# Kernel optimization log

Measured on AMD Instinct MI355X. Metric: run time of the kernel, lower is better.

The kernel has to match this reference:

```python
import jax, jax.numpy as jnp
import numpy as np

N = 1_000_000
C = 32
DIMS = (480, 360, 32)  # cylindrical voxel grid (z/rho, phi, height)
EPS = 1e-5


def setup_inputs() -> dict:
    rng = np.random.default_rng(0)
    total = DIMS[0] * DIMS[1] * DIMS[2]
    # unique active voxels, sorted so searchsorted gives row indices directly
    ids = np.sort(rng.choice(total, size=N, replace=False)).astype(np.int64)
    z = ids // (DIMS[1] * DIMS[2])
    rem = ids % (DIMS[1] * DIMS[2])
    y = rem // DIMS[2]
    x = rem % DIMS[2]
    coords = np.stack([z, y, x], axis=1)
    strides = np.array([DIMS[1] * DIMS[2], DIMS[2], 1], dtype=np.int64)

    def nbr(delta):
        out = np.full((3, N), -1, dtype=np.int32)
        for a in range(3):
            tgt = ids + delta * strides[a]
            ok = (coords[:, a] + delta >= 0) & (coords[:, a] + delta < DIMS[a])
            pos = np.searchsorted(ids, tgt)
            pos_c = np.clip(pos, 0, N - 1)
            found = ok & (ids[pos_c] == tgt)
            out[a] = np.where(found, pos_c, -1).astype(np.int32)
        return out

    nbr_prev = nbr(-1)
    nbr_next = nbr(+1)

    key = jax.random.key(0)
    k0, k1, k2 = jax.random.split(key, 3)
    features = jax.random.normal(k0, (N, C), dtype=jnp.float32)
    # W[branch, tap, in, out]; taps ordered (-1, 0, +1) along the branch's axis
    W = jax.random.normal(k1, (3, 3, C, C), dtype=jnp.float32) * (1.0 / np.sqrt(3 * C))
    gamma = jnp.ones((3, C), dtype=jnp.float32)
    beta = jnp.zeros((3, C), dtype=jnp.float32)
    mean = jax.random.normal(k2, (3, C), dtype=jnp.float32) * 0.1
    var = jnp.ones((3, C), dtype=jnp.float32)
    return {
        "features": features,
        "nbr_prev": jnp.asarray(nbr_prev),
        "nbr_next": jnp.asarray(nbr_next),
        "W": W,
        "gamma": gamma,
        "beta": beta,
        "mean": mean,
        "var": var,
    }


def _branch(f, Wb, prev, nxt, g, b, m, v):
    # 3-tap submanifold conv along one axis: gather prev/next active neighbors
    pm = prev >= 0
    nm = nxt >= 0
    fp = jnp.where(pm[:, None], f[jnp.where(pm, prev, 0)], 0.0)
    fn = jnp.where(nm[:, None], f[jnp.where(nm, nxt, 0)], 0.0)
    out = fp @ Wb[0] + f @ Wb[1] + fn @ Wb[2]
    # BatchNorm1d (inference stats) + Sigmoid
    out = (out - m) * (g * jax.lax.rsqrt(v + EPS)) + b
    return jax.nn.sigmoid(out)


def reference(features, nbr_prev, nbr_next, W, gamma, beta, mean, var):
    acc = jnp.zeros_like(features)
    for a in range(3):  # conv3x1x1, conv1x3x1, conv1x1x3
        acc = acc + _branch(features, W[a], nbr_prev[a], nbr_next[a],
                            gamma[a], beta[a], mean[a], var[a])
    return acc * features  # sparse_add then gating with input features
```

## Files before the change

kernel.cpp:

```cpp
#include <hip/hip_runtime.h>
#include <stdint.h>


typedef __attribute__((ext_vector_type(8))) __bf16 bf16x8;
typedef __attribute__((ext_vector_type(8))) unsigned short u16x8;
typedef __attribute__((ext_vector_type(4))) float f32x4;
typedef __attribute__((ext_vector_type(2))) float f32x2;

constexpr int NVOX    = 1000000;
constexpr int NTILES  = NVOX / 16;
constexpr int WPB     = 4;
constexpr float LOG2E = 1.4426950408889634f;

constexpr int TPWF     = 5;
constexpr int NWAVESF  = NTILES / TPWF;
constexpr int NBLOCKSF = NWAVESF / WPB;

constexpr int TPW2     = 2;
constexpr int NWAVES2  = (NTILES + TPW2 - 1) / TPW2;
constexpr int NBLOCKS2 = (NWAVES2 + WPB - 1) / WPB;

constexpr int    WS_WELEMS = 18 * 64 * 8;
constexpr size_t FB_BYTES  = (size_t)NVOX * 64;
constexpr unsigned ZOFF    = (unsigned)(FB_BYTES + 18432 + 768);
constexpr size_t WS_NEED   = FB_BYTES + 18432 + 768 + 128;

constexpr int CVT_THREADS = NVOX * 32 / 16;
constexpr int PREP_TAIL   = WS_WELEMS + 96 + 32;
constexpr int PREPALL_BLK = (CVT_THREADS + PREP_TAIL + 255) / 256;

__device__ __forceinline__ unsigned pack_bf(float a, float b) {
    union { float f; unsigned u; } ca, cb; ca.f = a; cb.f = b;
    return __builtin_amdgcn_perm(cb.u + 0x8000u, ca.u + 0x8000u, 0x07060302u);
}

__device__ __forceinline__ void prep_tail_work(
    int t, const float* __restrict__ Wt,
    const float* __restrict__ gma, const float* __restrict__ bta,
    const float* __restrict__ mea, const float* __restrict__ var,
    unsigned short* __restrict__ wsW, float* __restrict__ wsA,
    float* __restrict__ wsB, float* __restrict__ wsZ)
{
    if (t < WS_WELEMS) {
        int f    = t >> 9;
        int rem  = t & 511;
        int lane = rem >> 3;
        int j    = rem & 7;
        int br = f / 6, tap = (f >> 1) % 3, h = f & 1;
        int n = lane & 15, quad = lane >> 4;
        float w = Wt[((br * 3 + tap) * 32 + quad * 8 + j) * 32 + 2 * n + h];
        union { float f; unsigned u; } c; c.f = w;
        wsW[(f * 64 + lane) * 8 + j] = (unsigned short)((c.u + 0x8000u) >> 16);
    } else if (t < WS_WELEMS + 96) {
        int i = t - WS_WELEMS;
        float s = gma[i] * __frsqrt_rn(var[i] + 1e-5f);
        wsA[i] = -s * LOG2E;
        wsB[i] = (mea[i] * s - bta[i]) * LOG2E;
    } else if (wsZ != nullptr && t < WS_WELEMS + 96 + 32) {
        wsZ[t - WS_WELEMS - 96] = 0.0f;
    }
}

__global__ __launch_bounds__(256) void prep_all(
    const float* __restrict__ feat, unsigned short* __restrict__ fb,
    const float* __restrict__ Wt,
    const float* __restrict__ gma, const float* __restrict__ bta,
    const float* __restrict__ mea, const float* __restrict__ var,
    unsigned short* __restrict__ wsW, float* __restrict__ wsA,
    float* __restrict__ wsB, float* __restrict__ wsZ)
{
    int tid = blockIdx.x * 256 + threadIdx.x;
    if (tid < CVT_THREADS) {
        const f32x4* p = (const f32x4*)(feat + (size_t)tid * 16);
        f32x4 v0 = p[0], v1 = p[1], v2 = p[2], v3 = p[3];
        union { unsigned u[8]; u16x8 v[2]; } r;
        r.u[0] = pack_bf(v0[0], v0[1]); r.u[1] = pack_bf(v0[2], v0[3]);
        r.u[2] = pack_bf(v1[0], v1[1]); r.u[3] = pack_bf(v1[2], v1[3]);
        r.u[4] = pack_bf(v2[0], v2[1]); r.u[5] = pack_bf(v2[2], v2[3]);
        r.u[6] = pack_bf(v3[0], v3[1]); r.u[7] = pack_bf(v3[2], v3[3]);
        u16x8* q = (u16x8*)(fb + (size_t)tid * 16);
        q[0] = r.v[0]; q[1] = r.v[1];
    } else {
        prep_tail_work(tid - CVT_THREADS, Wt, gma, bta, mea, var,
                       wsW, wsA, wsB, wsZ);
    }
}

__global__ __launch_bounds__(256) void prep_kernel(
    const float* __restrict__ Wt,
    const float* __restrict__ gma, const float* __restrict__ bta,
    const float* __restrict__ mea, const float* __restrict__ var,
    unsigned short* __restrict__ wsW, float* __restrict__ wsA,
    float* __restrict__ wsB)
{
    int tid = blockIdx.x * 256 + threadIdx.x;
    prep_tail_work(tid, Wt, gma, bta, mea, var, wsW, wsA, wsB, nullptr);
}

__device__ __forceinline__ bf16x8 cvt_frag(f32x4 lo, f32x4 hi) {
    union { unsigned u[4]; bf16x8 v; } r;
    r.u[0] = pack_bf(lo[0], lo[1]); r.u[1] = pack_bf(lo[2], lo[3]);
    r.u[2] = pack_bf(hi[0], hi[1]); r.u[3] = pack_bf(hi[2], hi[3]);
    return r.v;
}

__device__ __forceinline__ f32x4 mfma16(u16x8 a, bf16x8 b, f32x4 c) {
    return __builtin_amdgcn_mfma_f32_16x16x32_bf16(
        __builtin_bit_cast(bf16x8, a), b, c, 0, 0, 0);
}

__global__ __launch_bounds__(256) void recon_bf16(
    const float* __restrict__ feat,
    const int*   __restrict__ nprev,
    const int*   __restrict__ nnext,
    const char*  __restrict__ fbc,
    const unsigned short* __restrict__ wsW,
    const float* __restrict__ wsA,
    const float* __restrict__ wsB,
    float*       __restrict__ out)
{
    __shared__ unsigned short smem[WS_WELEMS];
    {
        const u16x8* s = (const u16x8*)wsW;
        u16x8* d = (u16x8*)smem;
        #pragma unroll
        for (int i = 0; i < 5; ++i) {
            int k = (int)threadIdx.x + i * 256;
            if (k < 18 * 64) d[k] = s[k];
        }
    }
    __syncthreads();

    const int lane = threadIdx.x & 63;
    const int n    = lane & 15;
    const int quad = lane >> 4;
    const unsigned qo = (unsigned)quad * 16u;

    int b   = blockIdx.x;
    int per = NBLOCKSF / 8;
    int bs  = (b < per * 8) ? ((b & 7) * per + (b >> 3)) : b;
    int wv  = bs * WPB + (threadIdx.x >> 6);
    if (wv >= NWAVESF) return;
    const int t0 = wv * TPWF;

    f32x2 A_[3], B_[3];
    #pragma unroll
    for (int br = 0; br < 3; ++br) {
        A_[br] = *(const f32x2*)(wsA + br * 32 + 2 * n);
        B_[br] = *(const f32x2*)(wsB + br * 32 + 2 * n);
    }

    unsigned lbase = (unsigned)lane * 16u;

    int idxP[2][3], idxN[2][3];
    {
        int r0 = t0 * 16 + n;
        #pragma unroll
        for (int a = 0; a < 3; ++a) {
            idxP[0][a] = __builtin_nontemporal_load(nprev + a * NVOX + r0);
            idxN[0][a] = __builtin_nontemporal_load(nnext + a * NVOX + r0);
            idxP[1][a] = __builtin_nontemporal_load(nprev + a * NVOX + r0 + 16);
            idxN[1][a] = __builtin_nontemporal_load(nnext + a * NVOX + r0 + 16);
        }
    }

    u16x8 G[2][7];
    {
        int row0 = t0 * 16 + n;
        G[0][0] = *(const u16x8*)(fbc + (unsigned)row0 * 64u + qo);
        #pragma unroll
        for (int a = 0; a < 3; ++a) {
            unsigned op = idxP[0][a] >= 0 ? (unsigned)idxP[0][a] * 64u : ZOFF;
            unsigned on = idxN[0][a] >= 0 ? (unsigned)idxN[0][a] * 64u : ZOFF;
            G[0][1 + a] = *(const u16x8*)(fbc + op + qo);
            G[0][4 + a] = *(const u16x8*)(fbc + on + qo);
        }
    }

    #pragma unroll
    for (int tt = 0; tt < TPWF; ++tt) {
        const int cur  = tt & 1;
        const int nxt  = cur ^ 1;
        const int base = (t0 + tt) * 16;

        f32x2 fv[4];
        #pragma unroll
        for (int r = 0; r < 4; ++r)
            fv[r] = __builtin_nontemporal_load(
                (const f32x2*)(feat + (base + quad * 4 + r) * 32 + 2 * n));

        if (tt + 1 < TPWF) {
            int rown = base + 16 + n;
            G[nxt][0] = *(const u16x8*)(fbc + (unsigned)rown * 64u + qo);
            #pragma unroll
            for (int a = 0; a < 3; ++a) {
                unsigned op = idxP[nxt][a] >= 0 ? (unsigned)idxP[nxt][a] * 64u : ZOFF;
                unsigned on = idxN[nxt][a] >= 0 ? (unsigned)idxN[nxt][a] * 64u : ZOFF;
                G[nxt][1 + a] = *(const u16x8*)(fbc + op + qo);
                G[nxt][4 + a] = *(const u16x8*)(fbc + on + qo);
            }
        }
        if (tt + 2 < TPWF) {
            int r2 = base + 32 + n;
            #pragma unroll
            for (int a = 0; a < 3; ++a) {
                idxP[cur][a] = __builtin_nontemporal_load(nprev + a * NVOX + r2);
                idxN[cur][a] = __builtin_nontemporal_load(nnext + a * NVOX + r2);
            }
        }

        asm volatile("" : "+v"(lbase));
        const char* sb = (const char*)smem + lbase;

        f32x4 acc0 = {0.f, 0.f, 0.f, 0.f}, acc1 = {0.f, 0.f, 0.f, 0.f};
        #pragma unroll
        for (int br = 0; br < 3; ++br) {
            bf16x8 w0 = *(const bf16x8*)(sb + (br * 6 + 0) * 1024);
            bf16x8 w1 = *(const bf16x8*)(sb + (br * 6 + 1) * 1024);
            bf16x8 w2 = *(const bf16x8*)(sb + (br * 6 + 2) * 1024);
            bf16x8 w3 = *(const bf16x8*)(sb + (br * 6 + 3) * 1024);
            bf16x8 w4 = *(const bf16x8*)(sb + (br * 6 + 4) * 1024);
            bf16x8 w5 = *(const bf16x8*)(sb + (br * 6 + 5) * 1024);
            f32x4 c0 = {0.f, 0.f, 0.f, 0.f}, c1 = {0.f, 0.f, 0.f, 0.f};
            c0 = mfma16(G[cur][1 + br], w0, c0);
            c1 = mfma16(G[cur][1 + br], w1, c1);
            c0 = mfma16(G[cur][0],      w2, c0);
            c1 = mfma16(G[cur][0],      w3, c1);
            c0 = mfma16(G[cur][4 + br], w4, c0);
            c1 = mfma16(G[cur][4 + br], w5, c1);
            float a0 = A_[br][0], b0 = B_[br][0];
            float a1 = A_[br][1], b1 = B_[br][1];
            #pragma unroll
            for (int r = 0; r < 4; ++r) {
                float e0 = __builtin_amdgcn_exp2f(__builtin_fmaf(c0[r], a0, b0));
                float e1 = __builtin_amdgcn_exp2f(__builtin_fmaf(c1[r], a1, b1));
                acc0[r] += __builtin_amdgcn_rcpf(1.0f + e0);
                acc1[r] += __builtin_amdgcn_rcpf(1.0f + e1);
            }
        }

        #pragma unroll
        for (int r = 0; r < 4; ++r) {
            int vrow = base + quad * 4 + r;
            f32x2 ov = { acc0[r] * fv[r][0], acc1[r] * fv[r][1] };
            __builtin_nontemporal_store(ov, (f32x2*)(out + vrow * 32 + 2 * n));
        }
    }
}

__global__ __launch_bounds__(256) void recon_legacy(
    const float*          __restrict__ feat,
    const int*            __restrict__ nprev,
    const int*            __restrict__ nnext,
    const unsigned short* __restrict__ wsW,
    const float*          __restrict__ wsA,
    const float*          __restrict__ wsB,
    float*                __restrict__ out)
{
    const int lane = threadIdx.x & 63;
    const int n    = lane & 15;
    const int quad = lane >> 4;

    int b   = blockIdx.x;
    int per = NBLOCKS2 / 8;
    int bs  = (b < per * 8) ? ((b & 7) * per + (b >> 3)) : b;
    int wv  = bs * WPB + (threadIdx.x >> 6);

    const int t0 = wv * TPW2;
    if (t0 >= NTILES) return;

    bf16x8 Bf[18];
    #pragma unroll
    for (int f = 0; f < 18; ++f)
        Bf[f] = __builtin_bit_cast(bf16x8, *(const u16x8*)(wsW + (f * 64 + lane) * 8));

    f32x2 A_[3], B_[3];
    #pragma unroll
    for (int br = 0; br < 3; ++br) {
        A_[br] = *(const f32x2*)(wsA + br * 32 + 2 * n);
        B_[br] = *(const f32x2*)(wsB + br * 32 + 2 * n);
    }

    int ip[3], inx[3];
    {
        int row0 = t0 * 16 + n;
        #pragma unroll
        for (int a = 0; a < 3; ++a) {
            ip[a]  = nprev[a * NVOX + row0];
            inx[a] = nnext[a * NVOX + row0];
        }
    }

    #pragma unroll 1
    for (int tt = 0; tt < TPW2; ++tt) {
        int tile = t0 + tt;
        if (tile >= NTILES) break;
        int base = tile * 16;
        int row  = base + n;

        const f32x4* ps = (const f32x4*)(feat + row * 32 + quad * 8);
        f32x4 s_lo = ps[0], s_hi = ps[1];
        f32x4 p_lo[3], p_hi[3], n_lo[3], n_hi[3];
        #pragma unroll
        for (int a = 0; a < 3; ++a) {
            p_lo[a] = (f32x4){0.f, 0.f, 0.f, 0.f}; p_hi[a] = p_lo[a];
            n_lo[a] = p_lo[a];                     n_hi[a] = p_lo[a];
            if (ip[a] >= 0) {
                const f32x4* pp = (const f32x4*)(feat + ip[a] * 32 + quad * 8);
                p_lo[a] = pp[0]; p_hi[a] = pp[1];
            }
            if (inx[a] >= 0) {
                const f32x4* pn = (const f32x4*)(feat + inx[a] * 32 + quad * 8);
                n_lo[a] = pn[0]; n_hi[a] = pn[1];
            }
        }

        int ipn[3], inn[3];
        if (tt + 1 < TPW2 && tile + 1 < NTILES) {
            int nrow = row + 16;
            #pragma unroll
            for (int a = 0; a < 3; ++a) {
                ipn[a] = nprev[a * NVOX + nrow];
                inn[a] = nnext[a * NVOX + nrow];
            }
        } else {
            #pragma unroll
            for (int a = 0; a < 3; ++a) { ipn[a] = -1; inn[a] = -1; }
        }

        bf16x8 Aself = cvt_frag(s_lo, s_hi);
        bf16x8 Ap[3], An[3];
        #pragma unroll
        for (int a = 0; a < 3; ++a) {
            Ap[a] = cvt_frag(p_lo[a], p_hi[a]);
            An[a] = cvt_frag(n_lo[a], n_hi[a]);
        }

        f32x4 acc0 = {0.f, 0.f, 0.f, 0.f}, acc1 = {0.f, 0.f, 0.f, 0.f};
        #pragma unroll
        for (int br = 0; br < 3; ++br) {
            f32x4 c0 = {0.f, 0.f, 0.f, 0.f}, c1 = {0.f, 0.f, 0.f, 0.f};
            c0 = __builtin_amdgcn_mfma_f32_16x16x32_bf16(Ap[br], Bf[br*6 + 0], c0, 0, 0, 0);
            c1 = __builtin_amdgcn_mfma_f32_16x16x32_bf16(Ap[br], Bf[br*6 + 1], c1, 0, 0, 0);
            c0 = __builtin_amdgcn_mfma_f32_16x16x32_bf16(Aself,  Bf[br*6 + 2], c0, 0, 0, 0);
            c1 = __builtin_amdgcn_mfma_f32_16x16x32_bf16(Aself,  Bf[br*6 + 3], c1, 0, 0, 0);
            c0 = __builtin_amdgcn_mfma_f32_16x16x32_bf16(An[br], Bf[br*6 + 4], c0, 0, 0, 0);
            c1 = __builtin_amdgcn_mfma_f32_16x16x32_bf16(An[br], Bf[br*6 + 5], c1, 0, 0, 0);
            float a0 = A_[br][0], b0 = B_[br][0], a1 = A_[br][1], b1 = B_[br][1];
            #pragma unroll
            for (int r = 0; r < 4; ++r) {
                float e0 = __builtin_amdgcn_exp2f(__builtin_fmaf(c0[r], a0, b0));
                float e1 = __builtin_amdgcn_exp2f(__builtin_fmaf(c1[r], a1, b1));
                acc0[r] += __builtin_amdgcn_rcpf(1.0f + e0);
                acc1[r] += __builtin_amdgcn_rcpf(1.0f + e1);
            }
        }

        #pragma unroll
        for (int r = 0; r < 4; ++r) {
            int vrow = base + quad * 4 + r;
            f32x2 fv = *(const f32x2*)(feat + vrow * 32 + 2 * n);
            f32x2 ov = { acc0[r] * fv[0], acc1[r] * fv[1] };
            *(f32x2*)(out + vrow * 32 + 2 * n) = ov;
        }

        #pragma unroll
        for (int a = 0; a < 3; ++a) { ip[a] = ipn[a]; inx[a] = inn[a]; }
    }
}

extern "C" void kernel_launch(void* const* d_in, const int* in_sizes, int n_in,
                              void* d_out, int out_size, void* d_ws, size_t ws_size,
                              hipStream_t stream) {
    const float* feat  = (const float*)d_in[0];
    const int*   nprev = (const int*)d_in[1];
    const int*   nnext = (const int*)d_in[2];
    const float* Wt    = (const float*)d_in[3];
    const float* gma   = (const float*)d_in[4];
    const float* bta   = (const float*)d_in[5];
    const float* mea   = (const float*)d_in[6];
    const float* var   = (const float*)d_in[7];
    float*       o     = (float*)d_out;

    if (ws_size >= WS_NEED) {
        unsigned short* fb  = (unsigned short*)d_ws;
        unsigned short* wsW = (unsigned short*)((char*)d_ws + FB_BYTES);
        float* wsA = (float*)((char*)d_ws + FB_BYTES + 18432);
        float* wsB = wsA + 96;
        float* wsZ = wsB + 96;
        prep_all<<<PREPALL_BLK, 256, 0, stream>>>(
            feat, fb, Wt, gma, bta, mea, var, wsW, wsA, wsB, wsZ);
        recon_bf16<<<NBLOCKSF, 256, 0, stream>>>(feat, nprev, nnext,
            (const char*)d_ws, wsW, wsA, wsB, o);
    } else {
        unsigned short* wsW = (unsigned short*)d_ws;
        float* wsA = (float*)((char*)d_ws + WS_WELEMS * 2);
        float* wsB = wsA + 96;
        prep_kernel<<<(PREP_TAIL + 255) / 256, 256, 0, stream>>>(
            Wt, gma, bta, mea, var, wsW, wsA, wsB);
        recon_legacy<<<NBLOCKS2, 256, 0, stream>>>(feat, nprev, nnext,
                                                   wsW, wsA, wsB, o);
    }
}
```

Measured before the change: 305.9 us.

## Load all neighbor indices upfront, broadcast via shuffles, deepen gather prefetch to two tiles

The fused kernel now processes four tiles per wave instead of five. All 64 neighbor indices for the wave's four tiles are loaded once as coalesced per-lane reads and distributed with wave shuffles, rather than issued as repeated 16-lane nontemporal loads. The feature gather buffer becomes triple-buffered, so gathers are issued two tiles ahead. This trades more live registers (three sets of seven gathered vectors) for more memory latency hiding, and the grid grows with a rounded-up block count.

```diff
diff --git a/kernel.cpp b/kernel.cpp
--- a/kernel.cpp
+++ b/kernel.cpp
@@ -12,9 +12,9 @@
 constexpr int WPB     = 4;
 constexpr float LOG2E = 1.4426950408889634f;
 
-constexpr int TPWF     = 5;
+constexpr int TPWF     = 4;
 constexpr int NWAVESF  = NTILES / TPWF;
-constexpr int NBLOCKSF = NWAVESF / WPB;
+constexpr int NBLOCKSF = (NWAVESF + WPB - 1) / WPB;
 
 constexpr int TPW2     = 2;
 constexpr int NWAVES2  = (NTILES + TPW2 - 1) / TPW2;
@@ -152,35 +152,36 @@
 
     unsigned lbase = (unsigned)lane * 16u;
 
-    int idxP[2][3], idxN[2][3];
+    int pAll[3], nAll[3];
     {
-        int r0 = t0 * 16 + n;
-        #pragma unroll
-        for (int a = 0; a < 3; ++a) {
-            idxP[0][a] = __builtin_nontemporal_load(nprev + a * NVOX + r0);
-            idxN[0][a] = __builtin_nontemporal_load(nnext + a * NVOX + r0);
-            idxP[1][a] = __builtin_nontemporal_load(nprev + a * NVOX + r0 + 16);
-            idxN[1][a] = __builtin_nontemporal_load(nnext + a * NVOX + r0 + 16);
-        }
-    }
-
-    u16x8 G[2][7];
-    {
-        int row0 = t0 * 16 + n;
-        G[0][0] = *(const u16x8*)(fbc + (unsigned)row0 * 64u + qo);
-        #pragma unroll
-        for (int a = 0; a < 3; ++a) {
-            unsigned op = idxP[0][a] >= 0 ? (unsigned)idxP[0][a] * 64u : ZOFF;
-            unsigned on = idxN[0][a] >= 0 ? (unsigned)idxN[0][a] * 64u : ZOFF;
-            G[0][1 + a] = *(const u16x8*)(fbc + op + qo);
-            G[0][4 + a] = *(const u16x8*)(fbc + on + qo);
+        int r64 = t0 * 16 + lane;
+        #pragma unroll
+        for (int a = 0; a < 3; ++a) {
+            pAll[a] = nprev[a * NVOX + r64];
+            nAll[a] = nnext[a * NVOX + r64];
+        }
+    }
+
+    u16x8 G[3][7];
+    #pragma unroll
+    for (int tt = 0; tt < 2; ++tt) {
+        int row = t0 * 16 + tt * 16 + n;
+        G[tt][0] = *(const u16x8*)(fbc + (unsigned)row * 64u + qo);
+        #pragma unroll
+        for (int a = 0; a < 3; ++a) {
+            int ip = __shfl(pAll[a], tt * 16 + n, 64);
+            int in_ = __shfl(nAll[a], tt * 16 + n, 64);
+            unsigned op = ip >= 0 ? (unsigned)ip * 64u : ZOFF;
+            unsigned on = in_ >= 0 ? (unsigned)in_ * 64u : ZOFF;
+            G[tt][1 + a] = *(const u16x8*)(fbc + op + qo);
+            G[tt][4 + a] = *(const u16x8*)(fbc + on + qo);
         }
     }
 
     #pragma unroll
     for (int tt = 0; tt < TPWF; ++tt) {
-        const int cur  = tt & 1;
-        const int nxt  = cur ^ 1;
+        const int cur  = tt % 3;
+        const int pre  = (tt + 2) % 3;
         const int base = (t0 + tt) * 16;
 
         f32x2 fv[4];
@@ -189,23 +190,17 @@
             fv[r] = __builtin_nontemporal_load(
                 (const f32x2*)(feat + (base + quad * 4 + r) * 32 + 2 * n));
 
-        if (tt + 1 < TPWF) {
-            int rown = base + 16 + n;
-            G[nxt][0] = *(const u16x8*)(fbc + (unsigned)rown * 64u + qo);
+        if (tt + 2 < TPWF) {
+            int rown = base + 32 + n;
+            G[pre][0] = *(const u16x8*)(fbc + (unsigned)rown * 64u + qo);
             #pragma unroll
             for (int a = 0; a < 3; ++a) {
-                unsigned op = idxP[nxt][a] >= 0 ? (unsigned)idxP[nxt][a] * 64u : ZOFF;
-                unsigned on = idxN[nxt][a] >= 0 ? (unsigned)idxN[nxt][a] * 64u : ZOFF;
-                G[nxt][1 + a] = *(const u16x8*)(fbc + op + qo);
-                G[nxt][4 + a] = *(const u16x8*)(fbc + on + qo);
-            }
-        }
-        if (tt + 2 < TPWF) {
-            int r2 = base + 32 + n;
-            #pragma unroll
-            for (int a = 0; a < 3; ++a) {
-                idxP[cur][a] = __builtin_nontemporal_load(nprev + a * NVOX + r2);
-                idxN[cur][a] = __builtin_nontemporal_load(nnext + a * NVOX + r2);
+                int ip = __shfl(pAll[a], (tt + 2) * 16 + n, 64);
+                int in_ = __shfl(nAll[a], (tt + 2) * 16 + n, 64);
+                unsigned op = ip >= 0 ? (unsigned)ip * 64u : ZOFF;
+                unsigned on = in_ >= 0 ? (unsigned)in_ * 64u : ZOFF;
+                G[pre][1 + a] = *(const u16x8*)(fbc + op + qo);
+                G[pre][4 + a] = *(const u16x8*)(fbc + on + qo);
             }
         }
 
```

Measured after the change: 297.4 us. 2.8% less time.
